# Optimization experiments

Hardware: AMD Instinct MI355X
Metric: run time of the kernel (lower is better)

## Reference

```python
import jax, jax.numpy as jnp
import numpy as np

B, D, M = 512, 256, 256
TEMP = 0.07


def setup_inputs() -> dict:
    key = jax.random.key(0)
    k1, k2, k3, k4 = jax.random.split(key, 4)
    features_o = jax.random.normal(k1, (B, D), dtype=jnp.float32)
    features_i = jax.random.normal(k2, (B, D), dtype=jnp.float32)
    # 0/1 pos mask as float (used multiplicatively, like the torch code)
    mask = jax.random.randint(k3, (B, B), 0, 2).astype(jnp.float32)
    # fixed-length integer version of the boolean mask_sents selector
    mask_sents = jnp.sort(jax.random.randint(k4, (M,), 0, B)).astype(jnp.int64)
    return {"features_o": features_o, "features_i": features_i,
            "mask": mask, "mask_sents": mask_sents}


def reference(features_o, features_i, mask, mask_sents):
    # sub_type='pre', sim_type='dot', temperature=0.07
    anchor = features_o[mask_sents]                      # [M, D]
    sim = (anchor @ features_i.T) / TEMP                 # [M, B]
    mask_pos = mask[mask_sents]                          # [M, B]
    mask_neg = (1.0 - mask)[mask_sents]                  # [M, B]
    # ragged per-row pos x neg pairwise -logsigmoid, expressed densely with
    # the pos/neg masks as pair weights (zero rows contribute nothing,
    # matching the `if sent_pos_num > 0 and sent_neg_num > 0` guard)
    diff = sim[:, :, None] - sim[:, None, :]             # [M, B, B] pos - neg
    w = mask_pos[:, :, None] * mask_neg[:, None, :]      # [M, B, B]
    loss_sum = jnp.sum(-jax.nn.log_sigmoid(diff) * w)
    pair_num = jnp.sum(mask_pos.sum(1) * mask_neg.sum(1))
    loss = jnp.where(pair_num > 0, loss_sum / pair_num, loss_sum)
    return loss
```

## Files before the change

### kernel.cpp

```cpp
#include <hip/hip_runtime.h>
#include <hip/hip_bf16.h>


#define BDIM 512
#define MDIM 256
#define DDIM 256
#define INV_TEMP (1.0f / 0.07f)

__global__ __launch_bounds__(256) void sim_kernel(
        const float* __restrict__ fo, const float* __restrict__ fi,
        const int* __restrict__ sents, float* __restrict__ sim) {
    __shared__ float As[32][33];
    __shared__ float Bs[32][33];
    __shared__ int rowIdx[32];
    const int tid = threadIdx.x;
    const int m0 = blockIdx.y * 32;
    const int n0 = blockIdx.x * 32;
    if (tid < 32) rowIdx[tid] = sents[m0 + tid];
    __syncthreads();
    const int tx = tid & 15, ty = tid >> 4;
    float a00 = 0.f, a01 = 0.f, a10 = 0.f, a11 = 0.f;
    for (int k0 = 0; k0 < DDIM; k0 += 32) {
#pragma unroll
        for (int i = 0; i < 4; ++i) {
            int idx = tid + i * 256;
            int r = idx >> 5, c = idx & 31;
            As[r][c] = fo[rowIdx[r] * DDIM + k0 + c];
            Bs[r][c] = fi[(n0 + r) * DDIM + k0 + c];
        }
        __syncthreads();
#pragma unroll
        for (int k = 0; k < 32; ++k) {
            float av0 = As[ty][k],     av1 = As[ty + 16][k];
            float bv0 = Bs[tx][k],     bv1 = Bs[tx + 16][k];
            a00 = fmaf(av0, bv0, a00);
            a01 = fmaf(av0, bv1, a01);
            a10 = fmaf(av1, bv0, a10);
            a11 = fmaf(av1, bv1, a11);
        }
        __syncthreads();
    }
    sim[(m0 + ty) * BDIM + n0 + tx]           = a00 * INV_TEMP;
    sim[(m0 + ty) * BDIM + n0 + tx + 16]      = a01 * INV_TEMP;
    sim[(m0 + ty + 16) * BDIM + n0 + tx]      = a10 * INV_TEMP;
    sim[(m0 + ty + 16) * BDIM + n0 + tx + 16] = a11 * INV_TEMP;
}

__global__ __launch_bounds__(512) void loss_kernel(
        const float* __restrict__ sim, const float* __restrict__ mask,
        const int* __restrict__ sents, float* __restrict__ ws) {
    __shared__ float s_psim[BDIM];
    __shared__ float s_nsim[BDIM];
    __shared__ int s_wcnt[8];
    __shared__ float s_red[8];

    const int tid  = threadIdx.x;
    const int lane = tid & 63;
    const int wave = tid >> 6;
    const int m    = blockIdx.x >> 1;
    const int half = blockIdx.x & 1;

    const int srow = sents[m];
    const float simval = sim[m * BDIM + tid];
    const float mv = mask[srow * BDIM + tid];
    const bool flag = (mv > 0.5f);

    unsigned long long bal = __ballot(flag);
    int below = __popcll(bal & ((1ull << lane) - 1ull));
    if (lane == 0) s_wcnt[wave] = __popcll(bal);
    __syncthreads();
    int base_pos = 0, np = 0;
#pragma unroll
    for (int w = 0; w < 8; ++w) {
        int c = s_wcnt[w];
        if (w < wave) base_pos += c;
        np += c;
    }
    const int nn = BDIM - np;
    const int base_neg = wave * 64 - base_pos;
    if (flag) s_psim[base_pos + below]          = simval;
    else      s_nsim[base_neg + (lane - below)] = simval;
    __syncthreads();

    const int tn  = tid & 31;
    const int tp  = half * 16 + (tid >> 5);
    float acc = 0.f;
    if (np > 0 && nn > 0) {
        for (int jp = tp; jp < np; jp += 32) {
            const float sp = s_psim[jp];
            for (int jn = tn; jn < nn; jn += 32) {
                float x = s_nsim[jn] - sp;
                float e = __expf(-fabsf(x));
                acc += fmaxf(x, 0.f) + __logf(1.f + e);
            }
        }
    }

#pragma unroll
    for (int off = 32; off > 0; off >>= 1) acc += __shfl_down(acc, off);
    if (lane == 0) s_red[wave] = acc;
    __syncthreads();
    if (tid == 0) {
        float bs = 0.f;
#pragma unroll
        for (int w = 0; w < 8; ++w) bs += s_red[w];
        atomicAdd(&ws[0], bs);
        if (half == 0) atomicAdd((unsigned int*)ws + 1, (unsigned int)(np * nn));
    }
}

__global__ void finalize_kernel(const float* __restrict__ ws,
                                float* __restrict__ out) {
    float ls = ws[0];
    unsigned int pn = ((const unsigned int*)ws)[1];
    out[0] = (pn > 0u) ? (ls / (float)pn) : ls;
}

extern "C" void kernel_launch(void* const* d_in, const int* in_sizes, int n_in,
                              void* d_out, int out_size, void* d_ws, size_t ws_size,
                              hipStream_t stream) {
    const float* fo    = (const float*)d_in[0];
    const float* fi    = (const float*)d_in[1];
    const float* mask  = (const float*)d_in[2];
    const int*   sents = (const int*)d_in[3];
    float* out = (float*)d_out;

    float* ws  = (float*)d_ws;
    float* sim = (float*)((char*)d_ws + 256);

    hipMemsetAsync(d_ws, 0, 8, stream);

    dim3 grid1(BDIM / 32, MDIM / 32);
    sim_kernel<<<grid1, 256, 0, stream>>>(fo, fi, sents, sim);

    loss_kernel<<<2 * MDIM, 512, 0, stream>>>(sim, mask, sents, ws);

    finalize_kernel<<<1, 1, 0, stream>>>(ws, out);
}
```

Before: 90.79 us.

## Fuse similarity GEMV, pairwise loss and finalize into one kernel

Merges the tiled similarity GEMM, the pairwise loss kernel and the finalize kernel into a single launch. Each block computes its anchor row's similarities directly, with every thread doing a float4 dot product against one row of features_i. The last block, detected by an atomic counter, writes the final ratio. This removes two kernel launches and the sim round-trip through global memory. In exchange it drops the two-blocks-per-row split of the pairwise loop, halving the grid to 256 blocks, and each block rereads all of features_i with strided, uncoalesced per-thread row loads.

```diff
diff --git a/kernel.cpp b/kernel.cpp
--- a/kernel.cpp
+++ b/kernel.cpp
@@ -7,64 +7,41 @@
 #define DDIM 256
 #define INV_TEMP (1.0f / 0.07f)
 
-__global__ __launch_bounds__(256) void sim_kernel(
+__global__ __launch_bounds__(512) void fused_loss_kernel(
         const float* __restrict__ fo, const float* __restrict__ fi,
-        const int* __restrict__ sents, float* __restrict__ sim) {
-    __shared__ float As[32][33];
-    __shared__ float Bs[32][33];
-    __shared__ int rowIdx[32];
-    const int tid = threadIdx.x;
-    const int m0 = blockIdx.y * 32;
-    const int n0 = blockIdx.x * 32;
-    if (tid < 32) rowIdx[tid] = sents[m0 + tid];
-    __syncthreads();
-    const int tx = tid & 15, ty = tid >> 4;
-    float a00 = 0.f, a01 = 0.f, a10 = 0.f, a11 = 0.f;
-    for (int k0 = 0; k0 < DDIM; k0 += 32) {
-#pragma unroll
-        for (int i = 0; i < 4; ++i) {
-            int idx = tid + i * 256;
-            int r = idx >> 5, c = idx & 31;
-            As[r][c] = fo[rowIdx[r] * DDIM + k0 + c];
-            Bs[r][c] = fi[(n0 + r) * DDIM + k0 + c];
-        }
-        __syncthreads();
-#pragma unroll
-        for (int k = 0; k < 32; ++k) {
-            float av0 = As[ty][k],     av1 = As[ty + 16][k];
-            float bv0 = Bs[tx][k],     bv1 = Bs[tx + 16][k];
-            a00 = fmaf(av0, bv0, a00);
-            a01 = fmaf(av0, bv1, a01);
-            a10 = fmaf(av1, bv0, a10);
-            a11 = fmaf(av1, bv1, a11);
-        }
-        __syncthreads();
-    }
-    sim[(m0 + ty) * BDIM + n0 + tx]           = a00 * INV_TEMP;
-    sim[(m0 + ty) * BDIM + n0 + tx + 16]      = a01 * INV_TEMP;
-    sim[(m0 + ty + 16) * BDIM + n0 + tx]      = a10 * INV_TEMP;
-    sim[(m0 + ty + 16) * BDIM + n0 + tx + 16] = a11 * INV_TEMP;
-}
-
-__global__ __launch_bounds__(512) void loss_kernel(
-        const float* __restrict__ sim, const float* __restrict__ mask,
-        const int* __restrict__ sents, float* __restrict__ ws) {
+        const float* __restrict__ mask, const int* __restrict__ sents,
+        float* __restrict__ ws, float* __restrict__ out) {
+    __shared__ float s_anchor[DDIM];
     __shared__ float s_psim[BDIM];
     __shared__ float s_nsim[BDIM];
-    __shared__ int s_wcnt[8];
+    __shared__ int   s_wcnt[8];
     __shared__ float s_red[8];
 
     const int tid  = threadIdx.x;
     const int lane = tid & 63;
     const int wave = tid >> 6;
-    const int m    = blockIdx.x >> 1;
-    const int half = blockIdx.x & 1;
+    const int m    = blockIdx.x;
+    const int srow = sents[m];
 
-    const int srow = sents[m];
-    const float simval = sim[m * BDIM + tid];
+    if (tid < DDIM) s_anchor[tid] = fo[srow * DDIM + tid];
     const float mv = mask[srow * BDIM + tid];
+    __syncthreads();
+
+    const float4* bf = (const float4*)(fi + (size_t)tid * DDIM);
+    const float4* af = (const float4*)s_anchor;
+    float acc0 = 0.f, acc1 = 0.f;
+#pragma unroll 8
+    for (int k = 0; k < DDIM / 8; ++k) {
+        float4 b0 = bf[2 * k], b1 = bf[2 * k + 1];
+        float4 a0 = af[2 * k], a1 = af[2 * k + 1];
+        acc0 = fmaf(a0.x, b0.x, acc0); acc0 = fmaf(a0.y, b0.y, acc0);
+        acc0 = fmaf(a0.z, b0.z, acc0); acc0 = fmaf(a0.w, b0.w, acc0);
+        acc1 = fmaf(a1.x, b1.x, acc1); acc1 = fmaf(a1.y, b1.y, acc1);
+        acc1 = fmaf(a1.z, b1.z, acc1); acc1 = fmaf(a1.w, b1.w, acc1);
+    }
+    const float simval = (acc0 + acc1) * INV_TEMP;
+
     const bool flag = (mv > 0.5f);
-
     unsigned long long bal = __ballot(flag);
     int below = __popcll(bal & ((1ull << lane) - 1ull));
     if (lane == 0) s_wcnt[wave] = __popcll(bal);
@@ -82,38 +59,40 @@
     else      s_nsim[base_neg + (lane - below)] = simval;
     __syncthreads();
 
-    const int tn  = tid & 31;
-    const int tp  = half * 16 + (tid >> 5);
-    float acc = 0.f;
-    if (np > 0 && nn > 0) {
-        for (int jp = tp; jp < np; jp += 32) {
-            const float sp = s_psim[jp];
-            for (int jn = tn; jn < nn; jn += 32) {
-                float x = s_nsim[jn] - sp;
-                float e = __expf(-fabsf(x));
-                acc += fmaxf(x, 0.f) + __logf(1.f + e);
-            }
+    const int tn = tid & 31;
+    const int tp = tid >> 5;
+    float lsum = 0.f;
+    for (int jp = tp; jp < np; jp += 16) {
+        const float sp = s_psim[jp];
+        for (int jn = tn; jn < nn; jn += 32) {
+            float x = s_nsim[jn] - sp;
+            float e = __expf(-fabsf(x));
+            lsum += fmaxf(x, 0.f) + __logf(1.f + e);
         }
     }
 
 #pragma unroll
-    for (int off = 32; off > 0; off >>= 1) acc += __shfl_down(acc, off);
-    if (lane == 0) s_red[wave] = acc;
+    for (int off = 32; off > 0; off >>= 1) lsum += __shfl_down(lsum, off);
+    if (lane == 0) s_red[wave] = lsum;
     __syncthreads();
     if (tid == 0) {
         float bs = 0.f;
 #pragma unroll
         for (int w = 0; w < 8; ++w) bs += s_red[w];
         atomicAdd(&ws[0], bs);
-        if (half == 0) atomicAdd((unsigned int*)ws + 1, (unsigned int)(np * nn));
+        atomicAdd((unsigned int*)ws + 1, (unsigned int)(np * nn));
+        __threadfence();
+        unsigned int old = atomicAdd((unsigned int*)ws + 2, 1u);
+        if (old == (unsigned int)(gridDim.x - 1)) {
+            __threadfence();
+            float ls = __hip_atomic_load(&ws[0], __ATOMIC_RELAXED,
+                                         __HIP_MEMORY_SCOPE_AGENT);
+            unsigned int pn = __hip_atomic_load((unsigned int*)ws + 1,
+                                                __ATOMIC_RELAXED,
+                                                __HIP_MEMORY_SCOPE_AGENT);
+            out[0] = (pn > 0u) ? (ls / (float)pn) : ls;
+        }
     }
-}
-
-__global__ void finalize_kernel(const float* __restrict__ ws,
-                                float* __restrict__ out) {
-    float ls = ws[0];
-    unsigned int pn = ((const unsigned int*)ws)[1];
-    out[0] = (pn > 0u) ? (ls / (float)pn) : ls;
 }
 
 extern "C" void kernel_launch(void* const* d_in, const int* in_sizes, int n_in,
@@ -124,16 +103,9 @@
     const float* mask  = (const float*)d_in[2];
     const int*   sents = (const int*)d_in[3];
     float* out = (float*)d_out;
+    float* ws  = (float*)d_ws;
 
-    float* ws  = (float*)d_ws;
-    float* sim = (float*)((char*)d_ws + 256);
+    hipMemsetAsync(d_ws, 0, 12, stream);
 
-    hipMemsetAsync(d_ws, 0, 8, stream);
-
-    dim3 grid1(BDIM / 32, MDIM / 32);
-    sim_kernel<<<grid1, 256, 0, stream>>>(fo, fi, sents, sim);
-
-    loss_kernel<<<2 * MDIM, 512, 0, stream>>>(sim, mask, sents, ws);
-
-    finalize_kernel<<<1, 1, 0, stream>>>(ws, out);
+    fused_loss_kernel<<<MDIM, BDIM, 0, stream>>>(fo, fi, mask, sents, ws, out);
 }
```

After: 97.81 us. 7.7% more time.

## Register-block pairwise softplus in base-2 and fuse finalize into loss kernel

Applied to the files above, without the earlier changes.

Pre-scales sim by log2(e) so the pairwise softplus uses native exp2/log2 intrinsics, with a single ln2 multiply per block. Pos/neg values are loaded as float4 and padded with +/-inf sentinels, so each thread computes a 4x4 pair block and reuses its shared-memory loads. The grid grows to 4 blocks per row, and the finalize kernel is replaced by a last-block-done atomic counter. These changes cut transcendental cost, LDS traffic and one launch, at the price of more atomics and reliance on the infinite sentinels contributing exactly zero.

```diff
diff --git a/kernel.cpp b/kernel.cpp
--- a/kernel.cpp
+++ b/kernel.cpp
@@ -5,7 +5,9 @@
 #define BDIM 512
 #define MDIM 256
 #define DDIM 256
-#define INV_TEMP (1.0f / 0.07f)
+#define LOG2E 1.44269504088896340736f
+#define LN2   0.69314718055994530942f
+#define SIM_SCALE ((1.0f / 0.07f) * LOG2E)
 
 __global__ __launch_bounds__(256) void sim_kernel(
         const float* __restrict__ fo, const float* __restrict__ fi,
@@ -40,29 +42,32 @@
         }
         __syncthreads();
     }
-    sim[(m0 + ty) * BDIM + n0 + tx]           = a00 * INV_TEMP;
-    sim[(m0 + ty) * BDIM + n0 + tx + 16]      = a01 * INV_TEMP;
-    sim[(m0 + ty + 16) * BDIM + n0 + tx]      = a10 * INV_TEMP;
-    sim[(m0 + ty + 16) * BDIM + n0 + tx + 16] = a11 * INV_TEMP;
+    sim[(m0 + ty) * BDIM + n0 + tx]           = a00 * SIM_SCALE;
+    sim[(m0 + ty) * BDIM + n0 + tx + 16]      = a01 * SIM_SCALE;
+    sim[(m0 + ty + 16) * BDIM + n0 + tx]      = a10 * SIM_SCALE;
+    sim[(m0 + ty + 16) * BDIM + n0 + tx + 16] = a11 * SIM_SCALE;
 }
 
 __global__ __launch_bounds__(512) void loss_kernel(
         const float* __restrict__ sim, const float* __restrict__ mask,
-        const int* __restrict__ sents, float* __restrict__ ws) {
-    __shared__ float s_psim[BDIM];
-    __shared__ float s_nsim[BDIM];
-    __shared__ int s_wcnt[8];
+        const int* __restrict__ sents, float* __restrict__ ws,
+        float* __restrict__ out, int nblocks) {
+    __shared__ float4 s_psim4[130];
+    __shared__ float4 s_nsim4[130];
+    __shared__ int   s_wcnt[8];
     __shared__ float s_red[8];
+    float* s_psim = (float*)s_psim4;
+    float* s_nsim = (float*)s_nsim4;
 
     const int tid  = threadIdx.x;
     const int lane = tid & 63;
     const int wave = tid >> 6;
-    const int m    = blockIdx.x >> 1;
-    const int half = blockIdx.x & 1;
+    const int m    = blockIdx.x >> 2;
+    const int pblk = blockIdx.x & 3;
+    const int srow = sents[m];
 
-    const int srow = sents[m];
     const float simval = sim[m * BDIM + tid];
-    const float mv = mask[srow * BDIM + tid];
+    const float mv     = mask[srow * BDIM + tid];
     const bool flag = (mv > 0.5f);
 
     unsigned long long bal = __ballot(flag);
@@ -80,40 +85,57 @@
     const int base_neg = wave * 64 - base_pos;
     if (flag) s_psim[base_pos + below]          = simval;
     else      s_nsim[base_neg + (lane - below)] = simval;
+    if (tid < 4) {
+        s_psim[np + tid] =  __builtin_inff();
+        s_nsim[nn + tid] = -__builtin_inff();
+    }
     __syncthreads();
 
-    const int tn  = tid & 31;
-    const int tp  = half * 16 + (tid >> 5);
-    float acc = 0.f;
-    if (np > 0 && nn > 0) {
-        for (int jp = tp; jp < np; jp += 32) {
-            const float sp = s_psim[jp];
-            for (int jn = tn; jn < nn; jn += 32) {
-                float x = s_nsim[jn] - sp;
-                float e = __expf(-fabsf(x));
-                acc += fmaxf(x, 0.f) + __logf(1.f + e);
+    const int tn = tid & 31;
+    const int tp = tid >> 5;
+    const int p_t4 = (np + 3) >> 2;
+    const int n_t4 = (nn + 3) >> 2;
+    float lsum = 0.f;
+    for (int ip = pblk * 16 + tp; ip < p_t4; ip += 64) {
+        const float4 P = s_psim4[ip];
+        for (int in = tn; in < n_t4; in += 32) {
+            const float4 Nv = s_nsim4[in];
+#define SPLUS(nv, pv)                                                     \
+            {                                                             \
+                float t = (nv) - (pv);                                    \
+                float e = __builtin_amdgcn_exp2f(-__builtin_fabsf(t));    \
+                lsum += fmaxf(t, 0.f) + __builtin_amdgcn_logf(1.f + e);   \
             }
+            SPLUS(Nv.x, P.x) SPLUS(Nv.x, P.y) SPLUS(Nv.x, P.z) SPLUS(Nv.x, P.w)
+            SPLUS(Nv.y, P.x) SPLUS(Nv.y, P.y) SPLUS(Nv.y, P.z) SPLUS(Nv.y, P.w)
+            SPLUS(Nv.z, P.x) SPLUS(Nv.z, P.y) SPLUS(Nv.z, P.z) SPLUS(Nv.z, P.w)
+            SPLUS(Nv.w, P.x) SPLUS(Nv.w, P.y) SPLUS(Nv.w, P.z) SPLUS(Nv.w, P.w)
+#undef SPLUS
         }
     }
 
 #pragma unroll
-    for (int off = 32; off > 0; off >>= 1) acc += __shfl_down(acc, off);
-    if (lane == 0) s_red[wave] = acc;
+    for (int off = 32; off > 0; off >>= 1) lsum += __shfl_down(lsum, off);
+    if (lane == 0) s_red[wave] = lsum;
     __syncthreads();
     if (tid == 0) {
         float bs = 0.f;
 #pragma unroll
         for (int w = 0; w < 8; ++w) bs += s_red[w];
-        atomicAdd(&ws[0], bs);
-        if (half == 0) atomicAdd((unsigned int*)ws + 1, (unsigned int)(np * nn));
+        atomicAdd(&ws[0], bs * LN2);
+        if (pblk == 0) atomicAdd((unsigned int*)ws + 1, (unsigned int)(np * nn));
+        __threadfence();
+        unsigned int old = atomicAdd((unsigned int*)ws + 2, 1u);
+        if (old == (unsigned int)(nblocks - 1)) {
+            __threadfence();
+            float ls = __hip_atomic_load(&ws[0], __ATOMIC_RELAXED,
+                                         __HIP_MEMORY_SCOPE_AGENT);
+            unsigned int pn = __hip_atomic_load((unsigned int*)ws + 1,
+                                                __ATOMIC_RELAXED,
+                                                __HIP_MEMORY_SCOPE_AGENT);
+            out[0] = (pn > 0u) ? (ls / (float)pn) : ls;
+        }
     }
-}
-
-__global__ void finalize_kernel(const float* __restrict__ ws,
-                                float* __restrict__ out) {
-    float ls = ws[0];
-    unsigned int pn = ((const unsigned int*)ws)[1];
-    out[0] = (pn > 0u) ? (ls / (float)pn) : ls;
 }
 
 extern "C" void kernel_launch(void* const* d_in, const int* in_sizes, int n_in,
@@ -124,16 +146,14 @@
     const float* mask  = (const float*)d_in[2];
     const int*   sents = (const int*)d_in[3];
     float* out = (float*)d_out;
-
     float* ws  = (float*)d_ws;
     float* sim = (float*)((char*)d_ws + 256);
 
-    hipMemsetAsync(d_ws, 0, 8, stream);
+    hipMemsetAsync(d_ws, 0, 12, stream);
 
     dim3 grid1(BDIM / 32, MDIM / 32);
     sim_kernel<<<grid1, 256, 0, stream>>>(fo, fi, sents, sim);
 
-    loss_kernel<<<2 * MDIM, 512, 0, stream>>>(sim, mask, sents, ws);
-
-    finalize_kernel<<<1, 1, 0, stream>>>(ws, out);
+    const int nblocks = 4 * MDIM;
+    loss_kernel<<<nblocks, BDIM, 0, stream>>>(sim, mask, sents, ws, out, nblocks);
 }
```

Result: slower. 104.7 us (+15.4%).
